# Performance work log

Hardware: AMD Instinct MI355X
Metric: run time of the kernel (lower is better)

The kernel has to match this reference:

```python
import jax, jax.numpy as jnp
import numpy as np

N, E = 50000, 300000
NI, EI, H, OUT, L = 16, 8, 64, 3, 3  # node/edge input widths, hidden, output, conv_depth


def setup_inputs() -> dict:
    key = jax.random.key(0)
    ks = iter(jax.random.split(key, 64))
    def rn(shape, scale=0.05):
        return jax.random.normal(next(ks), shape, dtype=jnp.float32) * scale
    inp = {}
    inp["nodes"] = jax.random.normal(next(ks), (N, NI), dtype=jnp.float32)
    inp["edges"] = jax.random.normal(next(ks), (E, EI), dtype=jnp.float32)
    inp["edge_idx"] = jax.random.randint(next(ks), (E, 2), 0, N, dtype=jnp.int32)
    def mlp_params(prefix, din, lead=None):
        s = () if lead is None else (lead,)
        inp[prefix + "_W1"] = rn(s + (din, H))
        inp[prefix + "_b1"] = jnp.zeros(s + (H,), jnp.float32)
        inp[prefix + "_W2"] = rn(s + (H, H))
        inp[prefix + "_b2"] = jnp.zeros(s + (H,), jnp.float32)
        inp[prefix + "_g"] = jnp.ones(s + (H,), jnp.float32)
        inp[prefix + "_be"] = jnp.zeros(s + (H,), jnp.float32)
    mlp_params("ne", NI)            # node encoder
    mlp_params("ee", EI)            # edge encoder
    mlp_params("nm", 2 * H, lead=L)  # node messengers (stacked over conv_depth)
    mlp_params("em", 3 * H, lead=L)  # edge messengers
    inp["dec_W1"] = rn((H, H)); inp["dec_b1"] = jnp.zeros((H,), jnp.float32)
    inp["dec_W2"] = rn((H, OUT)); inp["dec_b2"] = jnp.zeros((OUT,), jnp.float32)
    return inp


def _lrelu(x):
    return jnp.where(x >= 0, x, 0.05 * x)


def _ln(x, g, b):
    m = jnp.mean(x, axis=-1, keepdims=True)
    v = jnp.mean((x - m) ** 2, axis=-1, keepdims=True)
    return (x - m) * jax.lax.rsqrt(v + 1e-5) * g + b


def _mlp(x, W1, b1, W2, b2, g, b):
    h = _lrelu(x @ W1 + b1)
    h = _lrelu(h @ W2 + b2)
    return _ln(h, g, b)


def reference(nodes, edges, edge_idx,
              ne_W1, ne_b1, ne_W2, ne_b2, ne_g, ne_be,
              ee_W1, ee_b1, ee_W2, ee_b2, ee_g, ee_be,
              nm_W1, nm_b1, nm_W2, nm_b2, nm_g, nm_be,
              em_W1, em_b1, em_W2, em_b2, em_g, em_be,
              dec_W1, dec_b1, dec_W2, dec_b2):
    n = _mlp(nodes, ne_W1, ne_b1, ne_W2, ne_b2, ne_g, ne_be)   # [N, H]
    e = _mlp(edges, ee_W1, ee_b1, ee_W2, ee_b2, ee_g, ee_be)   # [E, H]
    s, r = edge_idx[:, 0], edge_idx[:, 1]
    for i in range(L):
        e = e + _mlp(jnp.concatenate([e, n[s], n[r]], axis=1),
                     em_W1[i], em_b1[i], em_W2[i], em_b2[i], em_g[i], em_be[i])
        aggr = jax.ops.segment_sum(e, s, num_segments=n.shape[0])  # scatter_add onto senders
        n = n + _mlp(jnp.concatenate([n, aggr], axis=1),
                     nm_W1[i], nm_b1[i], nm_W2[i], nm_b2[i], nm_g[i], nm_be[i])
    h = _lrelu(n @ dec_W1 + dec_b1)
    return h @ dec_W2 + dec_b2  # [N, OUT]
```

## Files before the change

### kernel.cpp

```cpp
#include <hip/hip_runtime.h>

constexpr int BT = 256;

typedef __attribute__((ext_vector_type(8))) short short8v;
typedef __attribute__((ext_vector_type(4))) short short4v;
typedef __attribute__((ext_vector_type(4))) float f32x4;

__device__ __forceinline__ float lrelu(float x) { return x >= 0.f ? x : 0.05f * x; }

__device__ __forceinline__ unsigned short bf16_rne(float x) {
    unsigned u = __float_as_uint(x);
    u += 0x7FFFu + ((u >> 16) & 1u);
    return (unsigned short)(u >> 16);
}
__device__ __forceinline__ float bf16_to_f(unsigned short h) {
    return __uint_as_float(((unsigned)h) << 16);
}
__device__ __forceinline__ void split2(float x, unsigned short& hi, unsigned short& lo) {
    hi = bf16_rne(x);
    lo = bf16_rne(x - bf16_to_f(hi));
}


__device__ __forceinline__ void stageA64(const float* __restrict__ src, int row0, int nrows,
                                         short* __restrict__ A)
{
    for (int q = threadIdx.x; q < 1024; q += 256) {
        const int row = q >> 4;
        const int k0 = (q & 15) << 2;
        const int grow = row0 + row;
        float4 x = (grow < nrows) ? *reinterpret_cast<const float4*>(src + (long long)grow * 64 + k0)
                                  : make_float4(0.f, 0.f, 0.f, 0.f);
        unsigned short h0,h1,h2,h3,l0,l1,l2,l3;
        split2(x.x, h0, l0); split2(x.y, h1, l1); split2(x.z, h2, l2); split2(x.w, h3, l3);
        const int off = row * 64 + ((((k0 >> 3) ^ (row & 7))) << 3) + (k0 & 7);
        short4v hv; hv[0]=(short)h0; hv[1]=(short)h1; hv[2]=(short)h2; hv[3]=(short)h3;
        short4v lv; lv[0]=(short)l0; lv[1]=(short)l1; lv[2]=(short)l2; lv[3]=(short)l3;
        *reinterpret_cast<short4v*>(A + off) = hv;
        *reinterpret_cast<short4v*>(A + 4096 + off) = lv;
    }
}

__device__ __forceinline__ void gemm64(const short* __restrict__ A, const short* __restrict__ wf,
                                       int row, int g, int lane, f32x4* __restrict__ acc)
{
    #pragma unroll
    for (int s = 0; s < 2; ++s) {
        const int k8 = s * 4 + g;
        const int aoff = row * 64 + ((k8 ^ (row & 7)) << 3);
        const short8v a_hi = *reinterpret_cast<const short8v*>(A + aoff);
        const short8v a_lo = *reinterpret_cast<const short8v*>(A + 4096 + aoff);
        #pragma unroll
        for (int t = 0; t < 4; ++t) {
            const short8v b_hi = *reinterpret_cast<const short8v*>(wf + ((s*4+t)*2+0)*512 + lane*8);
            const short8v b_lo = *reinterpret_cast<const short8v*>(wf + ((s*4+t)*2+1)*512 + lane*8);
            acc[t] = __builtin_amdgcn_mfma_f32_16x16x32_bf16(a_hi, b_hi, acc[t], 0, 0, 0);
            acc[t] = __builtin_amdgcn_mfma_f32_16x16x32_bf16(a_lo, b_hi, acc[t], 0, 0, 0);
            acc[t] = __builtin_amdgcn_mfma_f32_16x16x32_bf16(a_hi, b_lo, acc[t], 0, 0, 0);
        }
    }
}

__global__ void k_prepw(const float* __restrict__ emW1, const float* __restrict__ emW2,
                        const float* __restrict__ nmW1, const float* __restrict__ nmW2,
                        const float* __restrict__ eeW2, const float* __restrict__ neW2,
                        const float* __restrict__ decW1,
                        short* __restrict__ wf)
{
    const int cid = blockIdx.x;
    const float* src;
    if (cid < 21) {
        const int layer = cid / 7, j = cid % 7;
        src =
            j == 0 ? emW1 + (size_t)layer * 12288 :
            j == 1 ? emW1 + (size_t)layer * 12288 + 4096 :
            j == 2 ? emW1 + (size_t)layer * 12288 + 8192 :
            j == 3 ? emW2 + (size_t)layer * 4096 :
            j == 4 ? nmW1 + (size_t)layer * 8192 :
            j == 5 ? nmW1 + (size_t)layer * 8192 + 4096 :
                     nmW2 + (size_t)layer * 4096;
    } else {
        src = (cid == 21) ? eeW2 : (cid == 22) ? neW2 : decW1;
    }
    short* dst = wf + (size_t)cid * 8192;
    for (int fr = threadIdx.x; fr < 1024; fr += 256) {
        const int lane = fr & 63;
        const int stp = fr >> 6;
        const int p = stp & 1;
        const int st = stp >> 1;
        const int s = st >> 2, t = st & 3;
        const int col = ((lane & 15) << 2) + t;
        const int k0 = s * 32 + (lane >> 4) * 8;
        short8v o;
        #pragma unroll
        for (int i = 0; i < 8; ++i) {
            const float w = src[(k0 + i) * 64 + col];
            const unsigned short hi = bf16_rne(w);
            o[i] = (short)(p ? bf16_rne(w - bf16_to_f(hi)) : hi);
        }
        *reinterpret_cast<short8v*>(dst + fr * 8) = o;
    }
}

template<int DIN, bool PERM>
__global__ __launch_bounds__(256) void k_enc_mf(
    const float* __restrict__ x, const int* __restrict__ csr,
    const float* __restrict__ W1, const float* __restrict__ b1,
    const short* __restrict__ wfW2, const float* __restrict__ b2,
    const float* __restrict__ gam, const float* __restrict__ bet,
    float* __restrict__ out, int nrows)
{
    __shared__ short Hf[8192];
    const int row0 = blockIdx.x * 64;
    const int lane = threadIdx.x & 63;
    const int wm = threadIdx.x >> 6;
    const int g = lane >> 4, c = lane & 15;
    const int c4 = c << 2;
    const int rowA = wm * 16 + c;

    long long orig[4];
    #pragma unroll
    for (int r = 0; r < 4; ++r) {
        const int grow = row0 + wm * 16 + g * 4 + r;
        orig[r] = (grow < nrows) ? (long long)(PERM ? csr[grow] : grow) : -1;
    }

    const f32x4 z4 = {0.f, 0.f, 0.f, 0.f};
    f32x4 acc[4];
    #pragma unroll
    for (int t = 0; t < 4; ++t) acc[t] = z4;

    #pragma unroll
    for (int kq = 0; kq < DIN / 4; ++kq) {
        float xv[4][4];
        #pragma unroll
        for (int r = 0; r < 4; ++r) {
            float4 t4 = make_float4(0.f, 0.f, 0.f, 0.f);
            if (orig[r] >= 0)
                t4 = *reinterpret_cast<const float4*>(x + orig[r] * DIN + kq * 4);
            xv[r][0] = t4.x; xv[r][1] = t4.y; xv[r][2] = t4.z; xv[r][3] = t4.w;
        }
        #pragma unroll
        for (int i = 0; i < 4; ++i) {
            const int k = kq * 4 + i;
            const float4 w4 = *reinterpret_cast<const float4*>(W1 + k * 64 + c4);
            const float wv[4] = {w4.x, w4.y, w4.z, w4.w};
            #pragma unroll
            for (int t = 0; t < 4; ++t)
                #pragma unroll
                for (int r = 0; r < 4; ++r)
                    acc[t][r] = fmaf(xv[r][i], wv[t], acc[t][r]);
        }
    }

    const float4 b1q = *reinterpret_cast<const float4*>(b1 + c4);
    const float b1a[4] = {b1q.x, b1q.y, b1q.z, b1q.w};
    #pragma unroll
    for (int r = 0; r < 4; ++r) {
        const int rl = wm * 16 + g * 4 + r;
        const int off = rl * 64 + (((c4 >> 3) ^ (rl & 7)) << 3) + (c4 & 7);
        short4v hv, lv;
        #pragma unroll
        for (int t = 0; t < 4; ++t) {
            const float h = lrelu(acc[t][r] + b1a[t]);
            unsigned short hi, lo; split2(h, hi, lo);
            hv[t] = (short)hi; lv[t] = (short)lo;
        }
        *reinterpret_cast<short4v*>(Hf + off) = hv;
        *reinterpret_cast<short4v*>(Hf + 4096 + off) = lv;
    }

    f32x4 acc2[4];
    #pragma unroll
    for (int t = 0; t < 4; ++t) acc2[t] = z4;
    gemm64(Hf, wfW2, rowA, g, lane, acc2);

    const float4 b2q = *reinterpret_cast<const float4*>(b2 + c4);
    const float b2a[4] = {b2q.x, b2q.y, b2q.z, b2q.w};
    #pragma unroll
    for (int t = 0; t < 4; ++t) {
        #pragma unroll
        for (int r = 0; r < 4; ++r) acc2[t][r] = lrelu(acc2[t][r] + b2a[t]);
    }
    const float4 gq = *reinterpret_cast<const float4*>(gam + c4);
    const float4 bq = *reinterpret_cast<const float4*>(bet + c4);
    const float gv[4] = {gq.x, gq.y, gq.z, gq.w};
    const float bv[4] = {bq.x, bq.y, bq.z, bq.w};
    #pragma unroll
    for (int r = 0; r < 4; ++r) {
        float s = acc2[0][r] + acc2[1][r] + acc2[2][r] + acc2[3][r];
        s += __shfl_xor(s, 1); s += __shfl_xor(s, 2); s += __shfl_xor(s, 4); s += __shfl_xor(s, 8);
        const float mu = s * 0.015625f;
        float q = 0.f;
        #pragma unroll
        for (int t = 0; t < 4; ++t) { const float d = acc2[t][r] - mu; q = fmaf(d, d, q); }
        q += __shfl_xor(q, 1); q += __shfl_xor(q, 2); q += __shfl_xor(q, 4); q += __shfl_xor(q, 8);
        const float rs = rsqrtf(q * 0.015625f + 1e-5f);
        const int grow = row0 + wm * 16 + g * 4 + r;
        if (grow < nrows) {
            float4 o;
            o.x = (acc2[0][r] - mu) * rs * gv[0] + bv[0];
            o.y = (acc2[1][r] - mu) * rs * gv[1] + bv[1];
            o.z = (acc2[2][r] - mu) * rs * gv[2] + bv[2];
            o.w = (acc2[3][r] - mu) * rs * gv[3] + bv[3];
            *reinterpret_cast<float4*>(out + (long long)grow * 64 + c4) = o;
        }
    }
}

__global__ __launch_bounds__(256) void k_uv_mf(
    const float* __restrict__ n, const short* __restrict__ wfB, const short* __restrict__ wfC,
    float* __restrict__ u, float* __restrict__ v, int N)
{
    __shared__ short Ab[8192];
    const int row0 = blockIdx.x * 64;
    stageA64(n, row0, N, Ab);
    __syncthreads();
    const int lane = threadIdx.x & 63;
    const int wm = threadIdx.x >> 6;
    const int g = lane >> 4, c = lane & 15;
    const int c4 = c << 2;
    const int rowA = wm * 16 + c;
    const f32x4 z4 = {0.f, 0.f, 0.f, 0.f};
    f32x4 acc[4];
    #pragma unroll
    for (int t = 0; t < 4; ++t) acc[t] = z4;
    gemm64(Ab, wfB, rowA, g, lane, acc);
    #pragma unroll
    for (int r = 0; r < 4; ++r) {
        const int grow = row0 + wm * 16 + g * 4 + r;
        if (grow < N) {
            float4 o; o.x = acc[0][r]; o.y = acc[1][r]; o.z = acc[2][r]; o.w = acc[3][r];
            *reinterpret_cast<float4*>(u + (long long)grow * 64 + c4) = o;
        }
    }
    #pragma unroll
    for (int t = 0; t < 4; ++t) acc[t] = z4;
    gemm64(Ab, wfC, rowA, g, lane, acc);
    #pragma unroll
    for (int r = 0; r < 4; ++r) {
        const int grow = row0 + wm * 16 + g * 4 + r;
        if (grow < N) {
            float4 o; o.x = acc[0][r]; o.y = acc[1][r]; o.z = acc[2][r]; o.w = acc[3][r];
            *reinterpret_cast<float4*>(v + (long long)grow * 64 + c4) = o;
        }
    }
}

__global__ __launch_bounds__(256) void k_edge_mf(
    float* __restrict__ e, const int* __restrict__ sp, const int* __restrict__ rp,
    const float* __restrict__ u, const float* __restrict__ v,
    const short* __restrict__ wfA, const short* __restrict__ wfW2,
    const float* __restrict__ b1, const float* __restrict__ b2,
    const float* __restrict__ gam, const float* __restrict__ bet, int E)
{
    __shared__ short Ab[8192];
    __shared__ short Hf[8192];
    const int row0 = blockIdx.x * 64;
    stageA64(e, row0, E, Ab);
    __syncthreads();
    const int lane = threadIdx.x & 63;
    const int wm = threadIdx.x >> 6;
    const int g = lane >> 4, c = lane & 15;
    const int c4 = c << 2;
    const int rowA = wm * 16 + c;
    int sidx[4], ridx[4];
    #pragma unroll
    for (int r = 0; r < 4; ++r) {
        const int grow = row0 + wm * 16 + g * 4 + r;
        if (grow < E) { sidx[r] = sp[grow]; ridx[r] = rp[grow]; }
        else          { sidx[r] = 0; ridx[r] = 0; }
    }
    const f32x4 z4 = {0.f, 0.f, 0.f, 0.f};
    f32x4 acc[4];
    #pragma unroll
    for (int t = 0; t < 4; ++t) acc[t] = z4;
    gemm64(Ab, wfA, rowA, g, lane, acc);

    const float4 b1q = *reinterpret_cast<const float4*>(b1 + c4);
    #pragma unroll
    for (int r = 0; r < 4; ++r) {
        const float4 uu = *reinterpret_cast<const float4*>(u + (long long)sidx[r] * 64 + c4);
        const float4 vv = *reinterpret_cast<const float4*>(v + (long long)ridx[r] * 64 + c4);
        acc[0][r] += b1q.x + uu.x + vv.x;
        acc[1][r] += b1q.y + uu.y + vv.y;
        acc[2][r] += b1q.z + uu.z + vv.z;
        acc[3][r] += b1q.w + uu.w + vv.w;
    }
    #pragma unroll
    for (int r = 0; r < 4; ++r) {
        const int rl = wm * 16 + g * 4 + r;
        const int off = rl * 64 + (((c4 >> 3) ^ (rl & 7)) << 3) + (c4 & 7);
        short4v hv, lv;
        #pragma unroll
        for (int t = 0; t < 4; ++t) {
            const float h = lrelu(acc[t][r]);
            unsigned short hi, lo; split2(h, hi, lo);
            hv[t] = (short)hi; lv[t] = (short)lo;
        }
        *reinterpret_cast<short4v*>(Hf + off) = hv;
        *reinterpret_cast<short4v*>(Hf + 4096 + off) = lv;
    }
    f32x4 acc2[4];
    #pragma unroll
    for (int t = 0; t < 4; ++t) acc2[t] = z4;
    gemm64(Hf, wfW2, rowA, g, lane, acc2);

    const float4 b2q = *reinterpret_cast<const float4*>(b2 + c4);
    const float b2a[4] = {b2q.x, b2q.y, b2q.z, b2q.w};
    #pragma unroll
    for (int t = 0; t < 4; ++t) {
        #pragma unroll
        for (int r = 0; r < 4; ++r) acc2[t][r] = lrelu(acc2[t][r] + b2a[t]);
    }
    const float4 gq = *reinterpret_cast<const float4*>(gam + c4);
    const float4 bq = *reinterpret_cast<const float4*>(bet + c4);
    const float gv[4] = {gq.x, gq.y, gq.z, gq.w};
    const float bv[4] = {bq.x, bq.y, bq.z, bq.w};
    #pragma unroll
    for (int r = 0; r < 4; ++r) {
        float s = acc2[0][r] + acc2[1][r] + acc2[2][r] + acc2[3][r];
        s += __shfl_xor(s, 1); s += __shfl_xor(s, 2); s += __shfl_xor(s, 4); s += __shfl_xor(s, 8);
        const float mu = s * 0.015625f;
        float q = 0.f;
        #pragma unroll
        for (int t = 0; t < 4; ++t) { const float d = acc2[t][r] - mu; q = fmaf(d, d, q); }
        q += __shfl_xor(q, 1); q += __shfl_xor(q, 2); q += __shfl_xor(q, 4); q += __shfl_xor(q, 8);
        const float rs = rsqrtf(q * 0.015625f + 1e-5f);
        const int rl = wm * 16 + g * 4 + r;
        const int grow = row0 + rl;
        if (grow < E) {
            const int off = rl * 64 + (((c4 >> 3) ^ (rl & 7)) << 3) + (c4 & 7);
            const short4v eh = *reinterpret_cast<const short4v*>(Ab + off);
            const short4v el = *reinterpret_cast<const short4v*>(Ab + 4096 + off);
            float4 o;
            o.x = (acc2[0][r] - mu) * rs * gv[0] + bv[0] + bf16_to_f((unsigned short)eh[0]) + bf16_to_f((unsigned short)el[0]);
            o.y = (acc2[1][r] - mu) * rs * gv[1] + bv[1] + bf16_to_f((unsigned short)eh[1]) + bf16_to_f((unsigned short)el[1]);
            o.z = (acc2[2][r] - mu) * rs * gv[2] + bv[2] + bf16_to_f((unsigned short)eh[2]) + bf16_to_f((unsigned short)el[2]);
            o.w = (acc2[3][r] - mu) * rs * gv[3] + bv[3] + bf16_to_f((unsigned short)eh[3]) + bf16_to_f((unsigned short)el[3]);
            *reinterpret_cast<float4*>(e + (long long)grow * 64 + c4) = o;
        }
    }
}

__global__ __launch_bounds__(256) void k_node_mf(
    float* __restrict__ n, const float* __restrict__ aggr,
    const short* __restrict__ wfW1a, const short* __restrict__ wfW1b, const short* __restrict__ wfW2,
    const float* __restrict__ b1, const float* __restrict__ b2,
    const float* __restrict__ gam, const float* __restrict__ bet, int N)
{
    __shared__ short An[8192];
    __shared__ short Aa[8192];
    __shared__ short Hf[8192];
    const int row0 = blockIdx.x * 64;
    stageA64(n, row0, N, An);
    stageA64(aggr, row0, N, Aa);
    __syncthreads();
    const int lane = threadIdx.x & 63;
    const int wm = threadIdx.x >> 6;
    const int g = lane >> 4, c = lane & 15;
    const int c4 = c << 2;
    const int rowA = wm * 16 + c;
    const f32x4 z4 = {0.f, 0.f, 0.f, 0.f};
    f32x4 acc[4];
    #pragma unroll
    for (int t = 0; t < 4; ++t) acc[t] = z4;
    gemm64(An, wfW1a, rowA, g, lane, acc);
    gemm64(Aa, wfW1b, rowA, g, lane, acc);

    const float4 b1q = *reinterpret_cast<const float4*>(b1 + c4);
    const float b1a[4] = {b1q.x, b1q.y, b1q.z, b1q.w};
    #pragma unroll
    for (int r = 0; r < 4; ++r) {
        const int rl = wm * 16 + g * 4 + r;
        const int off = rl * 64 + (((c4 >> 3) ^ (rl & 7)) << 3) + (c4 & 7);
        short4v hv, lv;
        #pragma unroll
        for (int t = 0; t < 4; ++t) {
            const float h = lrelu(acc[t][r] + b1a[t]);
            unsigned short hi, lo; split2(h, hi, lo);
            hv[t] = (short)hi; lv[t] = (short)lo;
        }
        *reinterpret_cast<short4v*>(Hf + off) = hv;
        *reinterpret_cast<short4v*>(Hf + 4096 + off) = lv;
    }
    f32x4 acc2[4];
    #pragma unroll
    for (int t = 0; t < 4; ++t) acc2[t] = z4;
    gemm64(Hf, wfW2, rowA, g, lane, acc2);

    const float4 b2q = *reinterpret_cast<const float4*>(b2 + c4);
    const float b2a[4] = {b2q.x, b2q.y, b2q.z, b2q.w};
    #pragma unroll
    for (int t = 0; t < 4; ++t) {
        #pragma unroll
        for (int r = 0; r < 4; ++r) acc2[t][r] = lrelu(acc2[t][r] + b2a[t]);
    }
    const float4 gq = *reinterpret_cast<const float4*>(gam + c4);
    const float4 bq = *reinterpret_cast<const float4*>(bet + c4);
    const float gv[4] = {gq.x, gq.y, gq.z, gq.w};
    const float bv[4] = {bq.x, bq.y, bq.z, bq.w};
    #pragma unroll
    for (int r = 0; r < 4; ++r) {
        float s = acc2[0][r] + acc2[1][r] + acc2[2][r] + acc2[3][r];
        s += __shfl_xor(s, 1); s += __shfl_xor(s, 2); s += __shfl_xor(s, 4); s += __shfl_xor(s, 8);
        const float mu = s * 0.015625f;
        float q = 0.f;
        #pragma unroll
        for (int t = 0; t < 4; ++t) { const float d = acc2[t][r] - mu; q = fmaf(d, d, q); }
        q += __shfl_xor(q, 1); q += __shfl_xor(q, 2); q += __shfl_xor(q, 4); q += __shfl_xor(q, 8);
        const float rs = rsqrtf(q * 0.015625f + 1e-5f);
        const int rl = wm * 16 + g * 4 + r;
        const int grow = row0 + rl;
        if (grow < N) {
            const int off = rl * 64 + (((c4 >> 3) ^ (rl & 7)) << 3) + (c4 & 7);
            const short4v nh = *reinterpret_cast<const short4v*>(An + off);
            const short4v nl = *reinterpret_cast<const short4v*>(An + 4096 + off);
            float4 o;
            o.x = (acc2[0][r] - mu) * rs * gv[0] + bv[0] + bf16_to_f((unsigned short)nh[0]) + bf16_to_f((unsigned short)nl[0]);
            o.y = (acc2[1][r] - mu) * rs * gv[1] + bv[1] + bf16_to_f((unsigned short)nh[1]) + bf16_to_f((unsigned short)nl[1]);
            o.z = (acc2[2][r] - mu) * rs * gv[2] + bv[2] + bf16_to_f((unsigned short)nh[2]) + bf16_to_f((unsigned short)nl[2]);
            o.w = (acc2[3][r] - mu) * rs * gv[3] + bv[3] + bf16_to_f((unsigned short)nh[3]) + bf16_to_f((unsigned short)nl[3]);
            *reinterpret_cast<float4*>(n + (long long)grow * 64 + c4) = o;
        }
    }
}

__global__ __launch_bounds__(256) void k_dec_mf(
    const float* __restrict__ n, const short* __restrict__ wfW1, const float* __restrict__ b1,
    const float* __restrict__ W2, const float* __restrict__ b2,
    float* __restrict__ out, int N)
{
    __shared__ short An[8192];
    __shared__ float hrow[4096];
    const int row0 = blockIdx.x * 64;
    stageA64(n, row0, N, An);
    __syncthreads();
    const int lane = threadIdx.x & 63;
    const int wm = threadIdx.x >> 6;
    const int g = lane >> 4, c = lane & 15;
    const int c4 = c << 2;
    const int rowA = wm * 16 + c;
    const f32x4 z4 = {0.f, 0.f, 0.f, 0.f};
    f32x4 acc[4];
    #pragma unroll
    for (int t = 0; t < 4; ++t) acc[t] = z4;
    gemm64(An, wfW1, rowA, g, lane, acc);
    const float4 b1q = *reinterpret_cast<const float4*>(b1 + c4);
    const float b1a[4] = {b1q.x, b1q.y, b1q.z, b1q.w};
    #pragma unroll
    for (int t = 0; t < 4; ++t) {
        const int col = c4 + t;
        #pragma unroll
        for (int r = 0; r < 4; ++r) {
            const int rl = wm * 16 + g * 4 + r;
            hrow[rl * 64 + (col ^ (rl & 31))] = lrelu(acc[t][r] + b1a[t]);
        }
    }
    __syncthreads();
    const int row = threadIdx.x >> 2, o = threadIdx.x & 3;
    if (o < 3 && row0 + row < N) {
        float s = b2[o];
        #pragma unroll 8
        for (int k = 0; k < 64; ++k)
            s = fmaf(hrow[row * 64 + (k ^ (row & 31))], W2[k * 3 + o], s);
        out[(long long)(row0 + row) * 3 + o] = s;
    }
}

__global__ void k_hist(const int* __restrict__ eidx, int* __restrict__ cnt, int E)
{
    int i = blockIdx.x * 256 + threadIdx.x;
    if (i < E) atomicAdd(&cnt[eidx[2 * i]], 1);
}

__global__ void k_scan1(const int* __restrict__ cnt, int* __restrict__ starts,
                        int* __restrict__ bsum, int n)
{
    __shared__ int sh[256];
    const int tid = threadIdx.x;
    const int i = blockIdx.x * 256 + tid;
    const int val = (i < n) ? cnt[i] : 0;
    sh[tid] = val; __syncthreads();
    for (int off = 1; off < 256; off <<= 1) {
        int t = (tid >= off) ? sh[tid - off] : 0;
        __syncthreads();
        sh[tid] += t;
        __syncthreads();
    }
    if (i < n) starts[i] = sh[tid] - val;
    if (tid == 255) bsum[blockIdx.x] = sh[255];
}

__global__ void k_scan2(int* __restrict__ bsum, int nb)
{
    __shared__ int sh[256];
    const int tid = threadIdx.x;
    const int val = (tid < nb) ? bsum[tid] : 0;
    sh[tid] = val; __syncthreads();
    for (int off = 1; off < 256; off <<= 1) {
        int t = (tid >= off) ? sh[tid - off] : 0;
        __syncthreads();
        sh[tid] += t;
        __syncthreads();
    }
    if (tid < nb) bsum[tid] = sh[tid] - val;
}

__global__ void k_scan3(int* __restrict__ starts, const int* __restrict__ bsum, int n)
{
    int i = blockIdx.x * 256 + threadIdx.x;
    if (i < n) starts[i] += bsum[blockIdx.x];
}

__global__ void k_scatter(const int* __restrict__ eidx, const int* __restrict__ starts,
                          int* __restrict__ cursor, int* __restrict__ csr,
                          int* __restrict__ sp, int* __restrict__ rp, int E)
{
    int i = blockIdx.x * 256 + threadIdx.x;
    if (i < E) {
        const int s = eidx[2 * i];
        const int p = atomicAdd(&cursor[s], 1);
        const int q = starts[s] + p;
        csr[q] = i;
        sp[q] = s;
        rp[q] = eidx[2 * i + 1];
    }
}

__global__ __launch_bounds__(256) void k_aggr(
    const float* __restrict__ e, const int* __restrict__ starts, const int* __restrict__ cnt,
    float* __restrict__ aggr, int N)
{
    const int node = blockIdx.x * 4 + (threadIdx.x >> 6);
    if (node >= N) return;
    const int j = threadIdx.x & 63;
    const int st = starts[node], en = st + cnt[node];
    float a = 0.f;
    for (int t = st; t < en; ++t)
        a += e[(long long)t * 64 + j];
    aggr[(long long)node * 64 + j] = a;
}

extern "C" void kernel_launch(void* const* d_in, const int* in_sizes, int n_in,
                              void* d_out, int out_size, void* d_ws, size_t ws_size,
                              hipStream_t stream)
{
    (void)in_sizes; (void)n_in; (void)out_size; (void)ws_size;
    constexpr int N = 50000, E = 300000, L = 3;

    const float* nodes = (const float*)d_in[0];
    const float* edges = (const float*)d_in[1];
    const int*   eidx  = (const int*)d_in[2];
    const float* neW1 = (const float*)d_in[3];
    const float* neb1 = (const float*)d_in[4];
    const float* neW2 = (const float*)d_in[5];
    const float* neb2 = (const float*)d_in[6];
    const float* neg  = (const float*)d_in[7];
    const float* nebe = (const float*)d_in[8];
    const float* eeW1 = (const float*)d_in[9];
    const float* eeb1 = (const float*)d_in[10];
    const float* eeW2 = (const float*)d_in[11];
    const float* eeb2 = (const float*)d_in[12];
    const float* eeg  = (const float*)d_in[13];
    const float* eebe = (const float*)d_in[14];
    const float* nmW1 = (const float*)d_in[15];
    const float* nmb1 = (const float*)d_in[16];
    const float* nmW2 = (const float*)d_in[17];
    const float* nmb2 = (const float*)d_in[18];
    const float* nmg  = (const float*)d_in[19];
    const float* nmbe = (const float*)d_in[20];
    const float* emW1 = (const float*)d_in[21];
    const float* emb1 = (const float*)d_in[22];
    const float* emW2 = (const float*)d_in[23];
    const float* emb2 = (const float*)d_in[24];
    const float* emg  = (const float*)d_in[25];
    const float* embe = (const float*)d_in[26];
    const float* decW1 = (const float*)d_in[27];
    const float* decb1 = (const float*)d_in[28];
    const float* decW2 = (const float*)d_in[29];
    const float* decb2 = (const float*)d_in[30];

    float* n   = (float*)d_ws;
    float* u   = n + (size_t)N * 64;
    float* v   = u + (size_t)N * 64;
    float* e   = v + (size_t)N * 64;
    int* cnt    = (int*)(e + (size_t)E * 64);
    int* starts = cnt + N;
    int* csr    = starts + N;
    int* bsum   = csr + E;
    int* cursor = bsum + 256;
    int* sp     = cursor + N;
    int* rp     = sp + E;
    short* wf   = (short*)(rp + E);

    const int nbN = (N + BT - 1) / BT;
    const int nbE = (E + BT - 1) / BT;
    const int nbN64 = (N + 63) / 64;
    const int nbE64 = (E + 63) / 64;

    const short* wfEE  = wf + (size_t)21 * 8192;
    const short* wfNE  = wf + (size_t)22 * 8192;
    const short* wfDec = wf + (size_t)23 * 8192;

    k_prepw<<<24, 256, 0, stream>>>(emW1, emW2, nmW1, nmW2, eeW2, neW2, decW1, wf);
    hipMemsetAsync(cnt, 0, (size_t)N * sizeof(int), stream);
    hipMemsetAsync(cursor, 0, (size_t)N * sizeof(int), stream);
    k_hist<<<nbE, 256, 0, stream>>>(eidx, cnt, E);
    k_scan1<<<nbN, 256, 0, stream>>>(cnt, starts, bsum, N);
    k_scan2<<<1, 256, 0, stream>>>(bsum, nbN);
    k_scan3<<<nbN, 256, 0, stream>>>(starts, bsum, N);
    k_scatter<<<nbE, 256, 0, stream>>>(eidx, starts, cursor, csr, sp, rp, E);

    k_enc_mf<16, false><<<nbN64, 256, 0, stream>>>(nodes, nullptr, neW1, neb1, wfNE,
                                                   neb2, neg, nebe, n, N);
    k_enc_mf<8, true><<<nbE64, 256, 0, stream>>>(edges, csr, eeW1, eeb1, wfEE,
                                                 eeb2, eeg, eebe, e, E);

    for (int i = 0; i < L; ++i) {
        const short* wl = wf + (size_t)i * 7 * 8192;
        k_uv_mf<<<nbN64, 256, 0, stream>>>(n, wl + 8192, wl + 2 * 8192, u, v, N);
        k_edge_mf<<<nbE64, 256, 0, stream>>>(e, sp, rp, u, v, wl, wl + 3 * 8192,
                                             emb1 + i * 64, emb2 + i * 64,
                                             emg + i * 64, embe + i * 64, E);
        k_aggr<<<(N + 3) / 4, 256, 0, stream>>>(e, starts, cnt, u, N);
        k_node_mf<<<nbN64, 256, 0, stream>>>(n, u, wl + 4 * 8192, wl + 5 * 8192, wl + 6 * 8192,
                                             nmb1 + i * 64, nmb2 + i * 64,
                                             nmg + i * 64, nmbe + i * 64, N);
    }
    k_dec_mf<<<nbN64, 256, 0, stream>>>(n, wfDec, decb1, decW2, decb2, (float*)d_out, N);
}
```

Baseline: 462.0 us.

## Alias hidden-layer LDS onto input tiles and prefetch edge gathers early

The edge kernel now writes its hidden activations into the same shared buffer as the staged edge tile, after first saving the residual values in registers. This halves its shared-memory footprint, and it adds a min-blocks launch bound so more blocks can be resident per CU. The sender and receiver gathers from u and v are issued before the tile is staged, so their global-memory latency overlaps the staging. The node and decoder kernels also alias their scratch buffers onto input tiles; the decoder needs an extra barrier for this. The added register-held values and the launch bound risk register pressure or spills.

```diff
diff --git a/kernel.cpp b/kernel.cpp
--- a/kernel.cpp
+++ b/kernel.cpp
@@ -247,7 +247,7 @@
     }
 }
 
-__global__ __launch_bounds__(256) void k_edge_mf(
+__global__ __launch_bounds__(256, 4) void k_edge_mf(
     float* __restrict__ e, const int* __restrict__ sp, const int* __restrict__ rp,
     const float* __restrict__ u, const float* __restrict__ v,
     const short* __restrict__ wfA, const short* __restrict__ wfW2,
@@ -255,15 +255,13 @@
     const float* __restrict__ gam, const float* __restrict__ bet, int E)
 {
     __shared__ short Ab[8192];
-    __shared__ short Hf[8192];
     const int row0 = blockIdx.x * 64;
-    stageA64(e, row0, E, Ab);
-    __syncthreads();
     const int lane = threadIdx.x & 63;
     const int wm = threadIdx.x >> 6;
     const int g = lane >> 4, c = lane & 15;
     const int c4 = c << 2;
     const int rowA = wm * 16 + c;
+
     int sidx[4], ridx[4];
     #pragma unroll
     for (int r = 0; r < 4; ++r) {
@@ -271,6 +269,16 @@
         if (grow < E) { sidx[r] = sp[grow]; ridx[r] = rp[grow]; }
         else          { sidx[r] = 0; ridx[r] = 0; }
     }
+    float4 uu[4], vv[4];
+    #pragma unroll
+    for (int r = 0; r < 4; ++r) {
+        uu[r] = *reinterpret_cast<const float4*>(u + (long long)sidx[r] * 64 + c4);
+        vv[r] = *reinterpret_cast<const float4*>(v + (long long)ridx[r] * 64 + c4);
+    }
+
+    stageA64(e, row0, E, Ab);
+    __syncthreads();
+
     const f32x4 z4 = {0.f, 0.f, 0.f, 0.f};
     f32x4 acc[4];
     #pragma unroll
@@ -280,17 +288,18 @@
     const float4 b1q = *reinterpret_cast<const float4*>(b1 + c4);
     #pragma unroll
     for (int r = 0; r < 4; ++r) {
-        const float4 uu = *reinterpret_cast<const float4*>(u + (long long)sidx[r] * 64 + c4);
-        const float4 vv = *reinterpret_cast<const float4*>(v + (long long)ridx[r] * 64 + c4);
-        acc[0][r] += b1q.x + uu.x + vv.x;
-        acc[1][r] += b1q.y + uu.y + vv.y;
-        acc[2][r] += b1q.z + uu.z + vv.z;
-        acc[3][r] += b1q.w + uu.w + vv.w;
-    }
+        acc[0][r] += b1q.x + uu[r].x + vv[r].x;
+        acc[1][r] += b1q.y + uu[r].y + vv[r].y;
+        acc[2][r] += b1q.z + uu[r].z + vv[r].z;
+        acc[3][r] += b1q.w + uu[r].w + vv[r].w;
+    }
+    short4v eh[4], el[4];
     #pragma unroll
     for (int r = 0; r < 4; ++r) {
         const int rl = wm * 16 + g * 4 + r;
         const int off = rl * 64 + (((c4 >> 3) ^ (rl & 7)) << 3) + (c4 & 7);
+        eh[r] = *reinterpret_cast<const short4v*>(Ab + off);
+        el[r] = *reinterpret_cast<const short4v*>(Ab + 4096 + off);
         short4v hv, lv;
         #pragma unroll
         for (int t = 0; t < 4; ++t) {
@@ -298,13 +307,13 @@
             unsigned short hi, lo; split2(h, hi, lo);
             hv[t] = (short)hi; lv[t] = (short)lo;
         }
-        *reinterpret_cast<short4v*>(Hf + off) = hv;
-        *reinterpret_cast<short4v*>(Hf + 4096 + off) = lv;
+        *reinterpret_cast<short4v*>(Ab + off) = hv;
+        *reinterpret_cast<short4v*>(Ab + 4096 + off) = lv;
     }
     f32x4 acc2[4];
     #pragma unroll
     for (int t = 0; t < 4; ++t) acc2[t] = z4;
-    gemm64(Hf, wfW2, rowA, g, lane, acc2);
+    gemm64(Ab, wfW2, rowA, g, lane, acc2);
 
     const float4 b2q = *reinterpret_cast<const float4*>(b2 + c4);
     const float b2a[4] = {b2q.x, b2q.y, b2q.z, b2q.w};
@@ -327,17 +336,13 @@
         for (int t = 0; t < 4; ++t) { const float d = acc2[t][r] - mu; q = fmaf(d, d, q); }
         q += __shfl_xor(q, 1); q += __shfl_xor(q, 2); q += __shfl_xor(q, 4); q += __shfl_xor(q, 8);
         const float rs = rsqrtf(q * 0.015625f + 1e-5f);
-        const int rl = wm * 16 + g * 4 + r;
-        const int grow = row0 + rl;
+        const int grow = row0 + wm * 16 + g * 4 + r;
         if (grow < E) {
-            const int off = rl * 64 + (((c4 >> 3) ^ (rl & 7)) << 3) + (c4 & 7);
-            const short4v eh = *reinterpret_cast<const short4v*>(Ab + off);
-            const short4v el = *reinterpret_cast<const short4v*>(Ab + 4096 + off);
             float4 o;
-            o.x = (acc2[0][r] - mu) * rs * gv[0] + bv[0] + bf16_to_f((unsigned short)eh[0]) + bf16_to_f((unsigned short)el[0]);
-            o.y = (acc2[1][r] - mu) * rs * gv[1] + bv[1] + bf16_to_f((unsigned short)eh[1]) + bf16_to_f((unsigned short)el[1]);
-            o.z = (acc2[2][r] - mu) * rs * gv[2] + bv[2] + bf16_to_f((unsigned short)eh[2]) + bf16_to_f((unsigned short)el[2]);
-            o.w = (acc2[3][r] - mu) * rs * gv[3] + bv[3] + bf16_to_f((unsigned short)eh[3]) + bf16_to_f((unsigned short)el[3]);
+            o.x = (acc2[0][r] - mu) * rs * gv[0] + bv[0] + bf16_to_f((unsigned short)eh[r][0]) + bf16_to_f((unsigned short)el[r][0]);
+            o.y = (acc2[1][r] - mu) * rs * gv[1] + bv[1] + bf16_to_f((unsigned short)eh[r][1]) + bf16_to_f((unsigned short)el[r][1]);
+            o.z = (acc2[2][r] - mu) * rs * gv[2] + bv[2] + bf16_to_f((unsigned short)eh[r][2]) + bf16_to_f((unsigned short)el[r][2]);
+            o.w = (acc2[3][r] - mu) * rs * gv[3] + bv[3] + bf16_to_f((unsigned short)eh[r][3]) + bf16_to_f((unsigned short)el[r][3]);
             *reinterpret_cast<float4*>(e + (long long)grow * 64 + c4) = o;
         }
     }
@@ -351,7 +356,6 @@
 {
     __shared__ short An[8192];
     __shared__ short Aa[8192];
-    __shared__ short Hf[8192];
     const int row0 = blockIdx.x * 64;
     stageA64(n, row0, N, An);
     stageA64(aggr, row0, N, Aa);
@@ -381,13 +385,13 @@
             unsigned short hi, lo; split2(h, hi, lo);
             hv[t] = (short)hi; lv[t] = (short)lo;
         }
-        *reinterpret_cast<short4v*>(Hf + off) = hv;
-        *reinterpret_cast<short4v*>(Hf + 4096 + off) = lv;
+        *reinterpret_cast<short4v*>(Aa + off) = hv;
+        *reinterpret_cast<short4v*>(Aa + 4096 + off) = lv;
     }
     f32x4 acc2[4];
     #pragma unroll
     for (int t = 0; t < 4; ++t) acc2[t] = z4;
-    gemm64(Hf, wfW2, rowA, g, lane, acc2);
+    gemm64(Aa, wfW2, rowA, g, lane, acc2);
 
     const float4 b2q = *reinterpret_cast<const float4*>(b2 + c4);
     const float b2a[4] = {b2q.x, b2q.y, b2q.z, b2q.w};
@@ -432,7 +436,7 @@
     float* __restrict__ out, int N)
 {
     __shared__ short An[8192];
-    __shared__ float hrow[4096];
+    float* hrow = reinterpret_cast<float*>(An);
     const int row0 = blockIdx.x * 64;
     stageA64(n, row0, N, An);
     __syncthreads();
@@ -448,6 +452,7 @@
     gemm64(An, wfW1, rowA, g, lane, acc);
     const float4 b1q = *reinterpret_cast<const float4*>(b1 + c4);
     const float b1a[4] = {b1q.x, b1q.y, b1q.z, b1q.w};
+    __syncthreads();
     #pragma unroll
     for (int t = 0; t < 4; ++t) {
         const int col = c4 + t;
```

After: 472.8 us. 1.02x slower.
